# Optimization experiments

Hardware: AMD Instinct MI355X
Metric: run time of the kernel (lower is better)

Reference implementation:

```python
import jax, jax.numpy as jnp
import numpy as np

N, E, D_IN, H, D_OUT = 50000, 1600000, 256, 128, 64


def setup_inputs() -> dict:
    key = jax.random.key(0)
    ks = jax.random.split(key, 8)
    x = jax.random.normal(ks[0], (N, D_IN), dtype=jnp.float32)
    edge_index = jax.random.randint(ks[1], (2, E), 0, N, dtype=jnp.int64)
    W1 = jax.random.normal(ks[2], (D_IN, H), dtype=jnp.float32) / np.float32(np.sqrt(D_IN))
    b1 = jnp.zeros((H,), jnp.float32)
    W2 = jax.random.normal(ks[3], (H, H), dtype=jnp.float32) / np.float32(np.sqrt(H))
    b2 = jnp.zeros((H,), jnp.float32)
    W3 = jax.random.normal(ks[4], (H, D_OUT), dtype=jnp.float32) / np.float32(np.sqrt(H))
    b3 = jnp.zeros((D_OUT,), jnp.float32)
    return {"x": x, "W1": W1, "b1": b1, "W2": W2, "b2": b2, "W3": W3, "b3": b3,
            "edge_index": edge_index}


def reference(x, W1, b1, W2, b2, W3, b3, edge_index):
    n = x.shape[0]
    # GCN: add self-loops, symmetric normalization D^{-1/2}(A+I)D^{-1/2}
    loop = jnp.arange(n, dtype=edge_index.dtype)
    src = jnp.concatenate([edge_index[0], loop])
    dst = jnp.concatenate([edge_index[1], loop])
    deg = jax.ops.segment_sum(jnp.ones_like(dst, x.dtype), dst, num_segments=n)
    dinv = jnp.where(deg > 0, jax.lax.rsqrt(deg), 0.0).astype(x.dtype)
    norm = dinv[src] * dinv[dst]  # [E+N]

    def gcn_layer(h, W, b):
        h = h @ W                                   # [N, F_out]
        msg = norm[:, None] * h[src]                # gather + scale, [E+N, F_out]
        return jax.ops.segment_sum(msg, dst, num_segments=n) + b

    h = jax.nn.relu(gcn_layer(x, W1, b1))
    h = jax.nn.relu(gcn_layer(h, W2, b2))
    return gcn_layer(h, W3, b3)
```

## Files before the change

### kernel.cpp

```cpp
#include <hip/hip_runtime.h>


constexpr int DIN = 256;
constexpr int HID = 128;
constexpr int DOUT = 64;
constexpr int MAXB = 1024;
constexpr int BSH = 6;
constexpr int EPB = 8192;

typedef unsigned short ushort_t;
typedef unsigned int uint_t;
typedef __attribute__((ext_vector_type(8))) short bf16x8;
typedef __attribute__((ext_vector_type(4))) float f32x4;

__device__ inline ushort_t f2bf(float f) {
  uint_t u = __float_as_uint(f);
  u += 0x7FFF + ((u >> 16) & 1);
  return (ushort_t)(u >> 16);
}
__device__ inline float bf2f(ushort_t b) {
  return __uint_as_float(((uint_t)b) << 16);
}

template <int SH>
__device__ inline uint_t ldrow32(const ushort_t* __restrict__ t, int c, uint_t lb) {
  return *(const uint_t*)((const char*)t + ((((uint_t)c) << SH) | lb));
}
template <int SH>
__device__ inline uint2 ldrow64(const ushort_t* __restrict__ t, int c, uint_t lb) {
  return *(const uint2*)((const char*)t + ((((uint_t)c) << SH) | lb));
}


__device__ inline void wprep_one(const float* __restrict__ W, ushort_t* __restrict__ Bhi,
                                 ushort_t* __restrict__ Blo, int K, int F, int i) {
  int k = i / F, nn = i % F;
  int t = nn >> 4, s = k >> 5, q = (k >> 3) & 3, j = k & 7;
  int lane = q * 16 + (nn & 15);
  int KS = K >> 5;
  size_t idx = (((size_t)t * KS + s) * 64 + (size_t)lane) * 8 + j;
  float w = W[i];
  ushort_t h = f2bf(w);
  float r = w - bf2f(h);
  Bhi[idx] = h;
  Blo[idx] = f2bf(r);
}


__global__ __launch_bounds__(256) void initprep_kernel(
    int* __restrict__ bucket_total, int iblocks,
    const float* __restrict__ W1, ushort_t* __restrict__ W1hi, ushort_t* __restrict__ W1lo,
    const float* __restrict__ W2, ushort_t* __restrict__ W2hi, ushort_t* __restrict__ W2lo,
    const float* __restrict__ W3, ushort_t* __restrict__ W3hi, ushort_t* __restrict__ W3lo) {
  if ((int)blockIdx.x < iblocks) {
    int i = blockIdx.x * 256 + threadIdx.x;
    if (i < MAXB) bucket_total[i] = 0;
  } else {
    int idx = ((int)blockIdx.x - iblocks) * 256 + threadIdx.x;
    constexpr int S1 = DIN * HID;
    constexpr int S2 = S1 + HID * HID;
    constexpr int S3 = S2 + HID * DOUT;
    if (idx < S1) wprep_one(W1, W1hi, W1lo, DIN, HID, idx);
    else if (idx < S2) wprep_one(W2, W2hi, W2lo, HID, HID, idx - S1);
    else if (idx < S3) wprep_one(W3, W3hi, W3lo, HID, DOUT, idx - S2);
  }
}


__global__ __launch_bounds__(256) void bin_kernel(const int* __restrict__ dst, int e,
    int nbuckets, int* __restrict__ bucket_total, int* __restrict__ block_base) {
  __shared__ int h[MAXB];
  int tid = threadIdx.x;
  for (int i = tid; i < nbuckets; i += 256) h[i] = 0;
  __syncthreads();
  int base = blockIdx.x * EPB;
  int end = min(base + EPB, e);
  for (int i = base + tid; i < end; i += 256) atomicAdd(&h[dst[i] >> BSH], 1);
  __syncthreads();
  for (int i = tid; i < nbuckets; i += 256) {
    int v = h[i];
    if (v) block_base[(size_t)blockIdx.x * nbuckets + i] = atomicAdd(&bucket_total[i], v);
  }
}


__global__ __launch_bounds__(256) void scan_buckets_kernel(const int* __restrict__ total,
    int* __restrict__ base, int nb) {
  __shared__ int sums[256];
  int t = threadIdx.x;
  int a[4];
  int ls = 0;
#pragma unroll
  for (int k = 0; k < 4; ++k) {
    int idx = t * 4 + k;
    a[k] = (idx < nb) ? total[idx] : 0;
    ls += a[k];
  }
  sums[t] = ls;
  __syncthreads();
  for (int off = 1; off < 256; off <<= 1) {
    int u = (t >= off) ? sums[t - off] : 0;
    __syncthreads();
    sums[t] += u;
    __syncthreads();
  }
  int run = sums[t] - ls;
#pragma unroll
  for (int k = 0; k < 4; ++k) {
    int idx = t * 4 + k;
    if (idx < nb) base[idx] = run;
    run += a[k];
  }
  if (t == 255) base[nb] = sums[255];
}


template <int K, int F, bool SCALE>
__device__ inline void gemm_mfma_dev(const float* __restrict__ X,
    const ushort_t* __restrict__ Bhi, const ushort_t* __restrict__ Blo,
    const float* __restrict__ dinv, ushort_t* __restrict__ T, int n, int bid) {
  constexpr int NT = F / 16;
  constexpr int KS = K / 32;
  int wave = threadIdx.x >> 6;
  int lane = threadIdx.x & 63;
  int q = lane >> 4;
  int m = lane & 15;
  int arow = bid * 64 + wave * 16 + m;
  bool valid = arow < n;
  const float* xrow = X + (size_t)arow * K;

  f32x4 acc[NT];
#pragma unroll
  for (int t = 0; t < NT; ++t) acc[t] = (f32x4){0.f, 0.f, 0.f, 0.f};

  for (int s = 0; s < KS; ++s) {
    float av[8];
    if (valid) {
      float4 u0 = *(const float4*)(xrow + s * 32 + q * 8);
      float4 u1 = *(const float4*)(xrow + s * 32 + q * 8 + 4);
      av[0] = u0.x; av[1] = u0.y; av[2] = u0.z; av[3] = u0.w;
      av[4] = u1.x; av[5] = u1.y; av[6] = u1.z; av[7] = u1.w;
    } else {
#pragma unroll
      for (int j = 0; j < 8; ++j) av[j] = 0.f;
    }
    bf16x8 ahi, alo;
#pragma unroll
    for (int j = 0; j < 8; ++j) {
      ushort_t h = f2bf(av[j]);
      ahi[j] = (short)h;
      alo[j] = (short)f2bf(av[j] - bf2f(h));
    }
#pragma unroll
    for (int t = 0; t < NT; ++t) {
      size_t boff = (((size_t)t * KS + s) * 64 + (size_t)lane) * 8;
      bf16x8 bh = *(const bf16x8*)(Bhi + boff);
      bf16x8 bl = *(const bf16x8*)(Blo + boff);
      acc[t] = __builtin_amdgcn_mfma_f32_16x16x32_bf16(ahi, bh, acc[t], 0, 0, 0);
      acc[t] = __builtin_amdgcn_mfma_f32_16x16x32_bf16(alo, bh, acc[t], 0, 0, 0);
      acc[t] = __builtin_amdgcn_mfma_f32_16x16x32_bf16(ahi, bl, acc[t], 0, 0, 0);
    }
  }

  int orow_base = bid * 64 + wave * 16 + q * 4;
#pragma unroll
  for (int r = 0; r < 4; ++r) {
    int orow = orow_base + r;
    if (orow >= n) continue;
    float sc = SCALE ? dinv[orow] : 1.0f;
    ushort_t* trow = T + (size_t)orow * F + m;
#pragma unroll
    for (int t = 0; t < NT; ++t) trow[t * 16] = f2bf(sc * acc[t][r]);
  }
}


__global__ __launch_bounds__(256) void fusedA2_kernel(
    const float* __restrict__ X, const ushort_t* __restrict__ Bhi,
    const ushort_t* __restrict__ Blo, ushort_t* __restrict__ T, int n, int gblocks,
    const int* __restrict__ src, const int* __restrict__ dst,
    const int* __restrict__ bucket_base, const int* __restrict__ block_base,
    uint_t* __restrict__ binned, int e, int nbuckets) {
  if ((int)blockIdx.x < gblocks) {
    gemm_mfma_dev<DIN, HID, false>(X, Bhi, Blo, nullptr, T, n, blockIdx.x);
  } else {
    __shared__ int rkh[MAXB];
    __shared__ int cbase[MAXB];
    int tid = threadIdx.x;
    int blk = (int)blockIdx.x - gblocks;
    for (int i = tid; i < nbuckets; i += 256) {
      rkh[i] = 0;
      cbase[i] = bucket_base[i] + block_base[(size_t)blk * nbuckets + i];
    }
    __syncthreads();
    int base = blk * EPB;
    int end = min(base + EPB, e);
    for (int i = base + tid; i < end; i += 256) {
      int d = dst[i];
      int s = src[i];
      int b = d >> BSH;
      int r = atomicAdd(&rkh[b], 1);
      binned[cbase[b] + r] = ((uint_t)d << 16) | (uint_t)s;
    }
  }
}


__global__ __launch_bounds__(256) void csr_kernel(const uint_t* __restrict__ binned,
    const int* __restrict__ bucket_base, int n, int* __restrict__ row_start,
    int* __restrict__ deg, float* __restrict__ dinv, int* __restrict__ col,
    ushort_t* __restrict__ Ta) {
  __shared__ int cnt[64];
  __shared__ int rk[64];
  __shared__ int rs[64];
  __shared__ float sdinv[64];
  __shared__ int ebs[2];
  int tid = threadIdx.x;
  int b = blockIdx.x;
  int node0 = b << BSH;
  if (tid < 64) { cnt[tid] = 0; rk[tid] = 0; }
  if (tid == 0) { ebs[0] = bucket_base[b]; ebs[1] = bucket_base[b + 1]; }
  __syncthreads();
  int ebase = ebs[0];
  int esz = ebs[1] - ebase;
  for (int i = tid; i < esz; i += 256)
    atomicAdd(&cnt[(int)(binned[ebase + i] >> 16) - node0], 1);
  __syncthreads();
  if (tid < 64) {
    int v = cnt[tid];
    int inc = v;
#pragma unroll
    for (int off = 1; off < 64; off <<= 1) {
      int u = __shfl_up(inc, off, 64);
      if (tid >= off) inc += u;
    }
    rs[tid] = inc - v;
    float di = rsqrtf((float)(v + 1));
    sdinv[tid] = di;
    int node = node0 + tid;
    if (node < n) {
      deg[node] = v + 1;
      dinv[node] = di;
      row_start[node] = ebase + (inc - v);
    }
  }
  __syncthreads();
  for (int i = tid; i < esz; i += 256) {
    uint_t p = binned[ebase + i];
    int l = (int)(p >> 16) - node0;
    int r = atomicAdd(&rk[l], 1);
    col[ebase + rs[l] + r] = (int)(p & 0xFFFFu);
  }
  int nrows = min(64, n - node0);
  if (nrows > 0) {
    uint4* tw = (uint4*)Ta + ((size_t)node0 << 4);
    int nv4 = nrows << 4;
    for (int i = tid; i < nv4; i += 256) {
      float sc = sdinv[i >> 4];
      uint4 w = tw[i];
      uint_t ww[4] = {w.x, w.y, w.z, w.w};
#pragma unroll
      for (int j = 0; j < 4; ++j) {
        float lo = sc * bf2f((ushort_t)(ww[j] & 0xFFFF));
        float hi = sc * bf2f((ushort_t)(ww[j] >> 16));
        ww[j] = (uint_t)f2bf(lo) | ((uint_t)f2bf(hi) << 16);
      }
      w.x = ww[0]; w.y = ww[1]; w.z = ww[2]; w.w = ww[3];
      tw[i] = w;
    }
  }
}


template <int FOUT>
__global__ __launch_bounds__(512) void spmm_gemm_kernel(
    const ushort_t* __restrict__ t, const int* __restrict__ row_start,
    const int* __restrict__ deg, const int* __restrict__ col,
    const float* __restrict__ dinv, const float* __restrict__ bias,
    const ushort_t* __restrict__ Bhi, const ushort_t* __restrict__ Blo,
    ushort_t* __restrict__ Tout, int n) {
  constexpr int FIN = 128;
  constexpr int NPB = 16;
  constexpr int LDW = FIN + 4;
  __shared__ float agg[NPB][LDW];
  int wave = threadIdx.x >> 6;
  int lane = threadIdx.x & 63;
  int nb0 = (int)blockIdx.x * NPB;

  {
    int half = lane >> 5;
    int hl = lane & 31;
    int ln = wave * 2 + half;
    int node = nb0 + ln;
    bool hv = node < n;
    int vnode = hv ? node : 0;
    int rs = row_start[vnode];
    int e  = hv ? (deg[vnode] - 1) : 0;
    float di = hv ? dinv[vnode] : 0.f;
    uint_t lb = (uint_t)hl << 3;

    float a0 = 0.f, a1 = 0.f, a2 = 0.f, a3 = 0.f;
    {
      uint2 s = ldrow64<8>(t, vnode, lb);
      a0 = bf2f((ushort_t)(s.x & 0xFFFF)); a1 = bf2f((ushort_t)(s.x >> 16));
      a2 = bf2f((ushort_t)(s.y & 0xFFFF)); a3 = bf2f((ushort_t)(s.y >> 16));
      if (!hv) { a0 = a1 = a2 = a3 = 0.f; }
    }
    int emax = max(e, __shfl_xor(e, 32));
    for (int k = 0; k < emax; k += 8) {
      int c[8];
      uint2 v[8];
#pragma unroll
      for (int j = 0; j < 8; ++j) c[j] = col[(k + j) < e ? (rs + k + j) : rs];
#pragma unroll
      for (int j = 0; j < 8; ++j) v[j] = ldrow64<8>(t, c[j], lb);
#pragma unroll
      for (int j = 0; j < 8; ++j) {
        if ((k + j) < e) {
          a0 += bf2f((ushort_t)(v[j].x & 0xFFFF));
          a1 += bf2f((ushort_t)(v[j].x >> 16));
          a2 += bf2f((ushort_t)(v[j].y & 0xFFFF));
          a3 += bf2f((ushort_t)(v[j].y >> 16));
        }
      }
    }
    float4 bb = *(const float4*)(bias + 4 * hl);
    float4 o;
    o.x = hv ? fmaxf(fmaf(di, a0, bb.x), 0.f) : 0.f;
    o.y = hv ? fmaxf(fmaf(di, a1, bb.y), 0.f) : 0.f;
    o.z = hv ? fmaxf(fmaf(di, a2, bb.z), 0.f) : 0.f;
    o.w = hv ? fmaxf(fmaf(di, a3, bb.w), 0.f) : 0.f;
    *(float4*)&agg[ln][4 * hl] = o;
  }
  __syncthreads();

  constexpr int NT = FOUT / 16;
  constexpr int KS = FIN / 32;
  if (wave < NT) {
    int q = lane >> 4, m = lane & 15;
    f32x4 acc = (f32x4){0.f, 0.f, 0.f, 0.f};
    const float* arow = &agg[m][0];
#pragma unroll
    for (int s = 0; s < KS; ++s) {
      float4 u0 = *(const float4*)(arow + s * 32 + q * 8);
      float4 u1 = *(const float4*)(arow + s * 32 + q * 8 + 4);
      float av[8];
      av[0] = u0.x; av[1] = u0.y; av[2] = u0.z; av[3] = u0.w;
      av[4] = u1.x; av[5] = u1.y; av[6] = u1.z; av[7] = u1.w;
      bf16x8 ahi, alo;
#pragma unroll
      for (int j = 0; j < 8; ++j) {
        ushort_t h = f2bf(av[j]);
        ahi[j] = (short)h;
        alo[j] = (short)f2bf(av[j] - bf2f(h));
      }
      size_t boff = (((size_t)wave * KS + s) * 64 + (size_t)lane) * 8;
      bf16x8 bh = *(const bf16x8*)(Bhi + boff);
      bf16x8 bl = *(const bf16x8*)(Blo + boff);
      acc = __builtin_amdgcn_mfma_f32_16x16x32_bf16(ahi, bh, acc, 0, 0, 0);
      acc = __builtin_amdgcn_mfma_f32_16x16x32_bf16(alo, bh, acc, 0, 0, 0);
      acc = __builtin_amdgcn_mfma_f32_16x16x32_bf16(ahi, bl, acc, 0, 0, 0);
    }
#pragma unroll
    for (int r = 0; r < 4; ++r) {
      int orow = nb0 + q * 4 + r;
      if (orow >= n) continue;
      float sc = dinv[orow];
      Tout[(size_t)orow * FOUT + wave * 16 + m] = f2bf(sc * acc[r]);
    }
  }
}


__global__ __launch_bounds__(256) void spmm64_kernel(const ushort_t* __restrict__ t,
    const int* __restrict__ row_start, const int* __restrict__ deg,
    const int* __restrict__ col, const float* __restrict__ dinv,
    const float* __restrict__ bias, float* __restrict__ out, int n) {
  int gw = (int)((blockIdx.x * 256u + threadIdx.x) >> 6);
  int lane = threadIdx.x & 63;
  int half = lane >> 5;
  int hl = lane & 31;
  int n0 = gw * 2;
  if (n0 >= n) return;
  int node = n0 + half;
  bool valid = node < n;
  int vnode = valid ? node : n0;
  int rs = row_start[vnode];
  int e  = valid ? (deg[vnode] - 1) : 0;
  float di = dinv[vnode];
  uint_t lb = (uint_t)hl << 2;

  uint_t su = ldrow32<7>(t, vnode, lb);
  float ax = bf2f((ushort_t)(su & 0xFFFF));
  float ay = bf2f((ushort_t)(su >> 16));

  for (int k = 0; k < e; k += 8) {
    int c[8];
    uint_t v[8];
#pragma unroll
    for (int j = 0; j < 8; ++j) c[j] = col[(k + j) < e ? (rs + k + j) : rs];
#pragma unroll
    for (int j = 0; j < 8; ++j) v[j] = ldrow32<7>(t, c[j], lb);
#pragma unroll
    for (int j = 0; j < 8; ++j) {
      if ((k + j) < e) {
        ax += bf2f((ushort_t)(v[j] & 0xFFFF));
        ay += bf2f((ushort_t)(v[j] >> 16));
      }
    }
  }
  if (valid) {
    float bx = bias[2 * hl], by = bias[2 * hl + 1];
    ax = fmaf(di, ax, bx);
    ay = fmaf(di, ay, by);
    float2 o;
    o.x = ax;
    o.y = ay;
    *(float2*)(out + (size_t)node * DOUT + 2 * hl) = o;
  }
}


extern "C" void kernel_launch(void* const* d_in, const int* in_sizes, int n_in,
                              void* d_out, int out_size, void* d_ws, size_t ws_size,
                              hipStream_t stream) {
  const float* x  = (const float*)d_in[0];
  const float* W1 = (const float*)d_in[1];
  const float* b1 = (const float*)d_in[2];
  const float* W2 = (const float*)d_in[3];
  const float* b2 = (const float*)d_in[4];
  const float* W3 = (const float*)d_in[5];
  const float* b3 = (const float*)d_in[6];
  const int* ei   = (const int*)d_in[7];

  int n = in_sizes[0] / DIN;
  int e = in_sizes[7] / 2;
  const int* src = ei;
  const int* dst = ei + e;

  char* ws = (char*)d_ws;
  size_t off = 0;
  auto alloc = [&](size_t bytes) -> void* {
    off = (off + 255) & ~(size_t)255;
    void* p = ws + off;
    off += bytes;
    return p;
  };
  int nbuckets = (n + 63) >> BSH;
  int nbin = (e + EPB - 1) / EPB;

  int*      bucket_total = (int*)alloc((size_t)MAXB * 4);
  int*      bucket_base  = (int*)alloc((size_t)(MAXB + 1) * 4);
  int*      block_base   = (int*)alloc((size_t)nbin * nbuckets * 4);
  uint_t*   binned       = (uint_t*)alloc((size_t)e * 4);
  int*      deg          = (int*)alloc((size_t)n * 4);
  float*    dinv         = (float*)alloc((size_t)n * 4);
  int*      row_start    = (int*)alloc((size_t)n * 4);
  int*      col          = (int*)alloc((size_t)e * 4);
  ushort_t* Ta           = (ushort_t*)alloc((size_t)n * HID * 2);
  ushort_t* Tb           = (ushort_t*)alloc((size_t)n * HID * 2);
  ushort_t* W1hi         = (ushort_t*)alloc((size_t)DIN * HID * 2);
  ushort_t* W1lo         = (ushort_t*)alloc((size_t)DIN * HID * 2);
  ushort_t* W2hi         = (ushort_t*)alloc((size_t)HID * HID * 2);
  ushort_t* W2lo         = (ushort_t*)alloc((size_t)HID * HID * 2);
  ushort_t* W3hi         = (ushort_t*)alloc((size_t)HID * DOUT * 2);
  ushort_t* W3lo         = (ushort_t*)alloc((size_t)HID * DOUT * 2);
  (void)ws_size;

  int gemm_blocks = (n + 63) / 64;
  int sg_blocks = (n + 15) / 16;
  int nwaves = (n + 1) / 2;
  int spmm_blocks = (nwaves + 3) / 4;
  constexpr int WPREP_TOTAL = DIN * HID + HID * HID + HID * DOUT;
  int wblocks = (WPREP_TOTAL + 255) / 256;
  int iblocks = MAXB / 256;

  initprep_kernel<<<iblocks + wblocks, 256, 0, stream>>>(
      bucket_total, iblocks,
      W1, W1hi, W1lo, W2, W2hi, W2lo, W3, W3hi, W3lo);
  bin_kernel<<<nbin, 256, 0, stream>>>(dst, e, nbuckets, bucket_total, block_base);
  scan_buckets_kernel<<<1, 256, 0, stream>>>(bucket_total, bucket_base, nbuckets);
  fusedA2_kernel<<<gemm_blocks + nbin, 256, 0, stream>>>(
      x, W1hi, W1lo, Ta, n, gemm_blocks,
      src, dst, bucket_base, block_base, binned, e, nbuckets);
  csr_kernel<<<nbuckets, 256, 0, stream>>>(binned, bucket_base, n, row_start,
                                           deg, dinv, col, Ta);

  spmm_gemm_kernel<HID><<<sg_blocks, 512, 0, stream>>>(
      Ta, row_start, deg, col, dinv, b1, W2hi, W2lo, Tb, n);
  spmm_gemm_kernel<DOUT><<<sg_blocks, 512, 0, stream>>>(
      Tb, row_start, deg, col, dinv, b2, W3hi, W3lo, Ta, n);
  spmm64_kernel<<<spmm_blocks, 256, 0, stream>>>(
      Ta, row_start, deg, col, dinv, b3, (float*)d_out, n);
}
```

Measured before the change: 330.4 us.

## Split fused SpMM+GEMM into feature-sliced aggregation and separate MFMA GEMM kernels

Replaces the fused aggregate-then-GEMM kernel for layers 2 and 3 with two kernels. The first is an aggregation kernel that splits the 128 features into 8 slices across blocks, with 8 lanes per node each gathering 4 bytes. It writes fp32 hidden activations to a new buffer using nontemporal loads and stores. The second is the existing tiled MFMA GEMM, which then consumes that buffer. The intent is better gather locality per slice, so each slice's working set fits in cache, and a more efficient dense GEMM. The cost is an extra fp32 round trip through global memory and two more launches, and the column index array is now read 8 times.

```diff
diff --git a/kernel.cpp b/kernel.cpp
--- a/kernel.cpp
+++ b/kernel.cpp
@@ -12,6 +12,7 @@
 typedef unsigned int uint_t;
 typedef __attribute__((ext_vector_type(8))) short bf16x8;
 typedef __attribute__((ext_vector_type(4))) float f32x4;
+typedef __attribute__((ext_vector_type(2))) float f32x2;
 
 __device__ inline ushort_t f2bf(float f) {
   uint_t u = __float_as_uint(f);
@@ -25,10 +26,6 @@
 template <int SH>
 __device__ inline uint_t ldrow32(const ushort_t* __restrict__ t, int c, uint_t lb) {
   return *(const uint_t*)((const char*)t + ((((uint_t)c) << SH) | lb));
-}
-template <int SH>
-__device__ inline uint2 ldrow64(const ushort_t* __restrict__ t, int c, uint_t lb) {
-  return *(const uint2*)((const char*)t + ((((uint_t)c) << SH) | lb));
 }
 
 
@@ -174,6 +171,13 @@
   }
 }
 
+template <int K, int F>
+__global__ __launch_bounds__(256) void gemm_mfma_kernel(const float* __restrict__ X,
+    const ushort_t* __restrict__ Bhi, const ushort_t* __restrict__ Blo,
+    const float* __restrict__ dinv, ushort_t* __restrict__ T, int n) {
+  gemm_mfma_dev<K, F, true>(X, Bhi, Blo, dinv, T, n, blockIdx.x);
+}
+
 
 __global__ __launch_bounds__(256) void fusedA2_kernel(
     const float* __restrict__ X, const ushort_t* __restrict__ Bhi,
@@ -272,102 +276,50 @@
 }
 
 
-template <int FOUT>
-__global__ __launch_bounds__(512) void spmm_gemm_kernel(
+__global__ __launch_bounds__(256) void aggf_kernel(
     const ushort_t* __restrict__ t, const int* __restrict__ row_start,
     const int* __restrict__ deg, const int* __restrict__ col,
     const float* __restrict__ dinv, const float* __restrict__ bias,
-    const ushort_t* __restrict__ Bhi, const ushort_t* __restrict__ Blo,
-    ushort_t* __restrict__ Tout, int n) {
-  constexpr int FIN = 128;
-  constexpr int NPB = 16;
-  constexpr int LDW = FIN + 4;
-  __shared__ float agg[NPB][LDW];
-  int wave = threadIdx.x >> 6;
-  int lane = threadIdx.x & 63;
-  int nb0 = (int)blockIdx.x * NPB;
-
-  {
-    int half = lane >> 5;
-    int hl = lane & 31;
-    int ln = wave * 2 + half;
-    int node = nb0 + ln;
-    bool hv = node < n;
-    int vnode = hv ? node : 0;
-    int rs = row_start[vnode];
-    int e  = hv ? (deg[vnode] - 1) : 0;
-    float di = hv ? dinv[vnode] : 0.f;
-    uint_t lb = (uint_t)hl << 3;
-
-    float a0 = 0.f, a1 = 0.f, a2 = 0.f, a3 = 0.f;
-    {
-      uint2 s = ldrow64<8>(t, vnode, lb);
-      a0 = bf2f((ushort_t)(s.x & 0xFFFF)); a1 = bf2f((ushort_t)(s.x >> 16));
-      a2 = bf2f((ushort_t)(s.y & 0xFFFF)); a3 = bf2f((ushort_t)(s.y >> 16));
-      if (!hv) { a0 = a1 = a2 = a3 = 0.f; }
-    }
-    int emax = max(e, __shfl_xor(e, 32));
-    for (int k = 0; k < emax; k += 8) {
-      int c[8];
-      uint2 v[8];
-#pragma unroll
-      for (int j = 0; j < 8; ++j) c[j] = col[(k + j) < e ? (rs + k + j) : rs];
-#pragma unroll
-      for (int j = 0; j < 8; ++j) v[j] = ldrow64<8>(t, c[j], lb);
-#pragma unroll
-      for (int j = 0; j < 8; ++j) {
-        if ((k + j) < e) {
-          a0 += bf2f((ushort_t)(v[j].x & 0xFFFF));
-          a1 += bf2f((ushort_t)(v[j].x >> 16));
-          a2 += bf2f((ushort_t)(v[j].y & 0xFFFF));
-          a3 += bf2f((ushort_t)(v[j].y >> 16));
-        }
+    float* __restrict__ Hf, int n) {
+  constexpr int NPB = 32;
+  int bid = (int)blockIdx.x;
+  int slice = bid & 7;
+  int grp = (int)threadIdx.x >> 3;
+  int u = threadIdx.x & 7;
+  int node = (bid >> 3) * NPB + grp;
+  bool hv = node < n;
+  int vnode = hv ? node : 0;
+  int rs = row_start[vnode];
+  int e  = hv ? deg[vnode] - 1 : 0;
+  float di = hv ? dinv[vnode] : 0.f;
+  uint_t lb = ((uint_t)slice << 5) | ((uint_t)u << 2);
+
+  uint_t sv = ldrow32<8>(t, vnode, lb);
+  float a0 = bf2f((ushort_t)(sv & 0xFFFF));
+  float a1 = bf2f((ushort_t)(sv >> 16));
+
+  for (int k = 0; k < e; k += 8) {
+    int c[8];
+    uint_t v[8];
+#pragma unroll
+    for (int j = 0; j < 8; ++j)
+      c[j] = __builtin_nontemporal_load(col + ((k + j) < e ? (rs + k + j) : rs));
+#pragma unroll
+    for (int j = 0; j < 8; ++j) v[j] = ldrow32<8>(t, c[j], lb);
+#pragma unroll
+    for (int j = 0; j < 8; ++j) {
+      if ((k + j) < e) {
+        a0 += bf2f((ushort_t)(v[j] & 0xFFFF));
+        a1 += bf2f((ushort_t)(v[j] >> 16));
       }
     }
-    float4 bb = *(const float4*)(bias + 4 * hl);
-    float4 o;
-    o.x = hv ? fmaxf(fmaf(di, a0, bb.x), 0.f) : 0.f;
-    o.y = hv ? fmaxf(fmaf(di, a1, bb.y), 0.f) : 0.f;
-    o.z = hv ? fmaxf(fmaf(di, a2, bb.z), 0.f) : 0.f;
-    o.w = hv ? fmaxf(fmaf(di, a3, bb.w), 0.f) : 0.f;
-    *(float4*)&agg[ln][4 * hl] = o;
-  }
-  __syncthreads();
-
-  constexpr int NT = FOUT / 16;
-  constexpr int KS = FIN / 32;
-  if (wave < NT) {
-    int q = lane >> 4, m = lane & 15;
-    f32x4 acc = (f32x4){0.f, 0.f, 0.f, 0.f};
-    const float* arow = &agg[m][0];
-#pragma unroll
-    for (int s = 0; s < KS; ++s) {
-      float4 u0 = *(const float4*)(arow + s * 32 + q * 8);
-      float4 u1 = *(const float4*)(arow + s * 32 + q * 8 + 4);
-      float av[8];
-      av[0] = u0.x; av[1] = u0.y; av[2] = u0.z; av[3] = u0.w;
-      av[4] = u1.x; av[5] = u1.y; av[6] = u1.z; av[7] = u1.w;
-      bf16x8 ahi, alo;
-#pragma unroll
-      for (int j = 0; j < 8; ++j) {
-        ushort_t h = f2bf(av[j]);
-        ahi[j] = (short)h;
-        alo[j] = (short)f2bf(av[j] - bf2f(h));
-      }
-      size_t boff = (((size_t)wave * KS + s) * 64 + (size_t)lane) * 8;
-      bf16x8 bh = *(const bf16x8*)(Bhi + boff);
-      bf16x8 bl = *(const bf16x8*)(Blo + boff);
-      acc = __builtin_amdgcn_mfma_f32_16x16x32_bf16(ahi, bh, acc, 0, 0, 0);
-      acc = __builtin_amdgcn_mfma_f32_16x16x32_bf16(alo, bh, acc, 0, 0, 0);
-      acc = __builtin_amdgcn_mfma_f32_16x16x32_bf16(ahi, bl, acc, 0, 0, 0);
-    }
-#pragma unroll
-    for (int r = 0; r < 4; ++r) {
-      int orow = nb0 + q * 4 + r;
-      if (orow >= n) continue;
-      float sc = dinv[orow];
-      Tout[(size_t)orow * FOUT + wave * 16 + m] = f2bf(sc * acc[r]);
-    }
+  }
+  if (hv) {
+    int f0 = slice * 16 + 2 * u;
+    f32x2 o;
+    o.x = fmaxf(fmaf(di, a0, bias[f0]), 0.f);
+    o.y = fmaxf(fmaf(di, a1, bias[f0 + 1]), 0.f);
+    __builtin_nontemporal_store(o, (f32x2*)(Hf + (size_t)node * HID + f0));
   }
 }
 
@@ -459,6 +411,7 @@
   int*      col          = (int*)alloc((size_t)e * 4);
   ushort_t* Ta           = (ushort_t*)alloc((size_t)n * HID * 2);
   ushort_t* Tb           = (ushort_t*)alloc((size_t)n * HID * 2);
+  float*    Hf           = (float*)alloc((size_t)n * HID * 4);
   ushort_t* W1hi         = (ushort_t*)alloc((size_t)DIN * HID * 2);
   ushort_t* W1lo         = (ushort_t*)alloc((size_t)DIN * HID * 2);
   ushort_t* W2hi         = (ushort_t*)alloc((size_t)HID * HID * 2);
@@ -468,7 +421,8 @@
   (void)ws_size;
 
   int gemm_blocks = (n + 63) / 64;
-  int sg_blocks = (n + 15) / 16;
+  int agg_groups = (n + 31) / 32;
+  int agg_blocks = agg_groups * 8;
   int nwaves = (n + 1) / 2;
   int spmm_blocks = (nwaves + 3) / 4;
   constexpr int WPREP_TOTAL = DIN * HID + HID * HID + HID * DOUT;
@@ -486,10 +440,14 @@
   csr_kernel<<<nbuckets, 256, 0, stream>>>(binned, bucket_base, n, row_start,
                                            deg, dinv, col, Ta);
 
-  spmm_gemm_kernel<HID><<<sg_blocks, 512, 0, stream>>>(
-      Ta, row_start, deg, col, dinv, b1, W2hi, W2lo, Tb, n);
-  spmm_gemm_kernel<DOUT><<<sg_blocks, 512, 0, stream>>>(
-      Tb, row_start, deg, col, dinv, b2, W3hi, W3lo, Ta, n);
+  aggf_kernel<<<agg_blocks, 256, 0, stream>>>(
+      Ta, row_start, deg, col, dinv, b1, Hf, n);
+  gemm_mfma_kernel<HID, HID><<<gemm_blocks, 256, 0, stream>>>(
+      Hf, W2hi, W2lo, dinv, Tb, n);
+  aggf_kernel<<<agg_blocks, 256, 0, stream>>>(
+      Tb, row_start, deg, col, dinv, b2, Hf, n);
+  gemm_mfma_kernel<HID, DOUT><<<gemm_blocks, 256, 0, stream>>>(
+      Hf, W3hi, W3lo, dinv, Ta, n);
   spmm64_kernel<<<spmm_blocks, 256, 0, stream>>>(
       Ta, row_start, deg, col, dinv, b3, (float*)d_out, n);
 }
```

Measured after the change: 740.7 us. 124% more time.
